# Kernel tuning notes

Measured on AMD Instinct MI355X. Metric: run time of the kernel, lower is better.

## Reference

```python
import jax, jax.numpy as jnp
import numpy as np

EPS = 1e-12  # matches torch.nn.functional.normalize default eps

def _l2_normalize(x):
    # F.normalize: x / max(||x||_2, eps)
    n = jnp.linalg.norm(x, axis=-1, keepdims=True)
    return x / jnp.maximum(n, EPS)

def setup_inputs() -> dict:
    key = jax.random.key(0)
    k_z, k_e = jax.random.split(key)
    B, N, D, K = 8, 4096, 64, 8192
    z = jax.random.normal(k_z, (B, N, D), dtype=jnp.float32)
    # nn.Embedding weight initialized uniform(-1/K, 1/K)
    embedding = jax.random.uniform(k_e, (K, D), dtype=jnp.float32,
                                   minval=-1.0 / K, maxval=1.0 / K)
    return {"z": z, "embedding": embedding, "temperature": 1.0}

def reference(z, embedding, temperature):
    z_norm = _l2_normalize(z)                      # (B,N,D)
    codebook = _l2_normalize(embedding)            # (K,D)
    sim = jnp.einsum('bnd,kd->bnk', z_norm, codebook)  # (B,N,K)
    dists = 1.0 - sim
    probs = jax.nn.softmax(-dists / temperature, axis=-1)  # (B,N,K)
    z_q = jnp.einsum('bnk,kd->bnd', probs, codebook)       # (B,N,D)
    return (probs, z_q)
```

## Files before the change

kernel.cpp:

```cpp
#include <hip/hip_runtime.h>
#include <hip/hip_bf16.h>


#define M_TOTAL 32768
#define KCODES  8192
#define DDIM    64
#define KSPLIT  4
#define KCHUNK  (KCODES / KSPLIT)

typedef __attribute__((ext_vector_type(8))) short bf16x8;
typedef __attribute__((ext_vector_type(4))) float f32x4;

__device__ inline unsigned short f2bf(float x) {
  union { float f; unsigned u; } v; v.f = x;
  unsigned r = v.u + 0x7FFFu + ((v.u >> 16) & 1u);
  return (unsigned short)(r >> 16);
}

__global__ __launch_bounds__(256) void norm_rows_kernel(
    const float* __restrict__ in, unsigned short* __restrict__ F,
    unsigned short* __restrict__ FT, int nrows) {
  int row = blockIdx.x * 4 + (threadIdx.x >> 6);
  int d = threadIdx.x & 63;
  if (row >= nrows) return;
  float x = in[(size_t)row * DDIM + d];
  float s = x * x;
  s += __shfl_xor(s, 1);  s += __shfl_xor(s, 2);  s += __shfl_xor(s, 4);
  s += __shfl_xor(s, 8);  s += __shfl_xor(s, 16); s += __shfl_xor(s, 32);
  float scale = 1.0f / fmaxf(sqrtf(s), 1e-12f);
  unsigned short b = f2bf(x * scale);
  {
    int blk = row >> 4, ml = row & 15;
    int h = d >> 5, g = (d >> 3) & 3, j = d & 7;
    F[((size_t)(blk * 2 + h)) * 512 + (g * 16 + ml) * 8 + j] = b;
  }
  if (FT) {
    int ds = d >> 4, dl = d & 15;
    int kb = row >> 5, kg = (row >> 3) & 3, kj = row & 7;
    FT[((size_t)(kb * 4 + ds)) * 512 + (kg * 16 + dl) * 8 + kj] = b;
  }
}

__global__ __launch_bounds__(512, 4) void passA_kernel(
    const unsigned short* __restrict__ FZn,
    const unsigned short* __restrict__ FCb,
    const unsigned short* __restrict__ FCbT,
    const float* __restrict__ tptr,
    float* __restrict__ Up,
    float* __restrict__ rsp) {
  __shared__ __align__(16) unsigned short sbuf[2][4096];
  __shared__ __align__(16) unsigned short etile[8][2][16 * 56];
  const int tid = threadIdx.x;
  const int w  = tid >> 6, l = tid & 63, g = l >> 4, ml = l & 15;
  const int rb = blockIdx.x & 127;
  const int ks = blockIdx.x >> 7;
  const int mA = rb * 256 + w * 32;
  const int mB = mA + 16;
  const int k0 = ks * KCHUNK;
  const float sc = 1.4426950408889634f / tptr[0];

  const unsigned short* fz = FZn + ((size_t)((rb * 16 + w * 2) * 2)) * 512;
  const bf16x8 zA0 = *(const bf16x8*)(fz + l * 8);
  const bf16x8 zA1 = *(const bf16x8*)(fz + 512 + l * 8);
  const bf16x8 zB0 = *(const bf16x8*)(fz + 1024 + l * 8);
  const bf16x8 zB1 = *(const bf16x8*)(fz + 1536 + l * 8);

  const f32x4 zero = {0.f, 0.f, 0.f, 0.f};
  f32x4 uaccA[4] = {zero, zero, zero, zero};
  f32x4 uaccB[4] = {zero, zero, zero, zero};
  float rsA = 0.f, rsB = 0.f;

  const unsigned short* gb = (tid < 256 ? FCb : FCbT) + (size_t)(tid & 255) * 8;
  bf16x8 stg = *(const bf16x8*)(gb + (size_t)k0 * 64);
  int cur = 0;

  const int NIT = KCHUNK / 32;
  for (int it = 0; it < NIT; ++it) {
    *(bf16x8*)&sbuf[cur][tid * 8] = stg;
    if (it + 1 < NIT)
      stg = *(const bf16x8*)(gb + (size_t)(k0 + (it + 1) * 32) * 64);
    __syncthreads();
    const unsigned short* sb = &sbuf[cur][0];
#pragma unroll
    for (int cs = 0; cs < 2; ++cs) {
      const bf16x8 c0 = *(const bf16x8*)(sb + cs * 1024 + l * 8);
      const bf16x8 c1 = *(const bf16x8*)(sb + cs * 1024 + 512 + l * 8);
      f32x4 aA = __builtin_amdgcn_mfma_f32_16x16x32_bf16(c0, zA0, zero, 0, 0, 0);
      aA = __builtin_amdgcn_mfma_f32_16x16x32_bf16(c1, zA1, aA, 0, 0, 0);
      f32x4 aB = __builtin_amdgcn_mfma_f32_16x16x32_bf16(c0, zB0, zero, 0, 0, 0);
      aB = __builtin_amdgcn_mfma_f32_16x16x32_bf16(c1, zB1, aB, 0, 0, 0);
      float eA0 = exp2f((aA[0] - 1.0f) * sc), eA1 = exp2f((aA[1] - 1.0f) * sc);
      float eA2 = exp2f((aA[2] - 1.0f) * sc), eA3 = exp2f((aA[3] - 1.0f) * sc);
      float eB0 = exp2f((aB[0] - 1.0f) * sc), eB1 = exp2f((aB[1] - 1.0f) * sc);
      float eB2 = exp2f((aB[2] - 1.0f) * sc), eB3 = exp2f((aB[3] - 1.0f) * sc);
      rsA += (eA0 + eA1) + (eA2 + eA3);
      rsB += (eB0 + eB1) + (eB2 + eB3);
      union { __hip_bfloat162 h[2]; uint2 u; } pA, pB;
      pA.h[0] = __float22bfloat162_rn(make_float2(eA0, eA1));
      pA.h[1] = __float22bfloat162_rn(make_float2(eA2, eA3));
      pB.h[0] = __float22bfloat162_rn(make_float2(eB0, eB1));
      pB.h[1] = __float22bfloat162_rn(make_float2(eB2, eB3));
      *(uint2*)&etile[w][0][ml * 56 + cs * 16 + g * 4] = pA.u;
      *(uint2*)&etile[w][1][ml * 56 + cs * 16 + g * 4] = pB.u;
    }
    asm volatile("s_waitcnt lgkmcnt(0)" ::: "memory");
    const bf16x8 efA = *(const bf16x8*)&etile[w][0][ml * 56 + g * 8];
    const bf16x8 efB = *(const bf16x8*)&etile[w][1][ml * 56 + g * 8];
#pragma unroll
    for (int ds = 0; ds < 4; ++ds) {
      const bf16x8 ct = *(const bf16x8*)(sb + 2048 + ds * 512 + l * 8);
      uaccA[ds] = __builtin_amdgcn_mfma_f32_16x16x32_bf16(ct, efA, uaccA[ds], 0, 0, 0);
      uaccB[ds] = __builtin_amdgcn_mfma_f32_16x16x32_bf16(ct, efB, uaccB[ds], 0, 0, 0);
    }
    cur ^= 1;
  }

  rsA += __shfl_xor(rsA, 16);  rsA += __shfl_xor(rsA, 32);
  rsB += __shfl_xor(rsB, 16);  rsB += __shfl_xor(rsB, 32);
  if (g == 0) {
    rsp[(size_t)ks * M_TOTAL + mA + ml] = rsA;
    rsp[(size_t)ks * M_TOTAL + mB + ml] = rsB;
  }

  float* urA = Up + ((size_t)ks * M_TOTAL + mA + ml) * DDIM;
  float* urB = Up + ((size_t)ks * M_TOTAL + mB + ml) * DDIM;
#pragma unroll
  for (int ds = 0; ds < 4; ++ds) {
    *(f32x4*)(urA + ds * 16 + g * 4) = uaccA[ds];
    *(f32x4*)(urB + ds * 16 + g * 4) = uaccB[ds];
  }
}

__global__ __launch_bounds__(256) void rszq_kernel(
    const float* __restrict__ Up, const float* __restrict__ rsp,
    float* __restrict__ rs, float* __restrict__ zq) {
  size_t i = (size_t)blockIdx.x * 256 + threadIdx.x;
  int m = (int)(i >> 4);
  float s = rsp[m] + rsp[M_TOTAL + m] + rsp[2 * M_TOTAL + m] + rsp[3 * M_TOTAL + m];
  if ((i & 15) == 0) rs[m] = s;
  f32x4 u = *(const f32x4*)(Up + i * 4);
#pragma unroll
  for (int ks = 1; ks < KSPLIT; ++ks) {
    f32x4 p = *(const f32x4*)(Up + (size_t)ks * M_TOTAL * DDIM + i * 4);
#pragma unroll
    for (int r = 0; r < 4; ++r) u[r] += p[r];
  }
  float inv = 1.0f / s;
  f32x4 v = {u[0] * inv, u[1] * inv, u[2] * inv, u[3] * inv};
  *(f32x4*)(zq + i * 4) = v;
}

__global__ __launch_bounds__(512, 4) void probs_kernel(
    const unsigned short* __restrict__ FZn,
    const unsigned short* __restrict__ FCb,
    const float* __restrict__ tptr,
    const float* __restrict__ rsv,
    float* __restrict__ probs) {
  __shared__ __align__(16) unsigned short sbuf[2][4096];
  const int tid = threadIdx.x;
  const int w  = tid >> 6, l = tid & 63, g = l >> 4, ml = l & 15;
  const int rb = blockIdx.x & 255;
  const int ks = blockIdx.x >> 8;
  const int m_base = rb * 128 + w * 16;
  const int k0 = ks * KCHUNK;
  const float sc = 1.4426950408889634f / tptr[0];

  const unsigned short* fz = FZn + ((size_t)((rb * 8 + w) * 2)) * 512;
  const bf16x8 zn0 = *(const bf16x8*)(fz + l * 8);
  const bf16x8 zn1 = *(const bf16x8*)(fz + 512 + l * 8);
  const float inv = 1.0f / rsv[m_base + ml];
  const f32x4 zero = {0.f, 0.f, 0.f, 0.f};
  float* prow = probs + (size_t)(m_base + ml) * KCODES;

  const unsigned short* gb = FCb + (size_t)tid * 8;
  bf16x8 stg = *(const bf16x8*)(gb + (size_t)k0 * 64);
  int cur = 0;

  const int NIT = KCHUNK / 64;
  for (int it = 0; it < NIT; ++it) {
    *(bf16x8*)&sbuf[cur][tid * 8] = stg;
    if (it + 1 < NIT)
      stg = *(const bf16x8*)(gb + (size_t)(k0 + (it + 1) * 64) * 64);
    __syncthreads();
    const unsigned short* sb = &sbuf[cur][0];
    const int kc = k0 + it * 64;
#pragma unroll
    for (int cb = 0; cb < 4; ++cb) {
      const bf16x8 c0 = *(const bf16x8*)(sb + (cb * 2 + 0) * 512 + l * 8);
      const bf16x8 c1 = *(const bf16x8*)(sb + (cb * 2 + 1) * 512 + l * 8);
      f32x4 a = __builtin_amdgcn_mfma_f32_16x16x32_bf16(c0, zn0, zero, 0, 0, 0);
      a = __builtin_amdgcn_mfma_f32_16x16x32_bf16(c1, zn1, a, 0, 0, 0);
      f32x4 p;
#pragma unroll
      for (int r = 0; r < 4; ++r) p[r] = exp2f((a[r] - 1.0f) * sc) * inv;
      *(f32x4*)(prow + kc + cb * 16 + g * 4) = p;
    }
    cur ^= 1;
  }
}

extern "C" void kernel_launch(void* const* d_in, const int* in_sizes, int n_in,
                              void* d_out, int out_size, void* d_ws, size_t ws_size,
                              hipStream_t stream) {
  const float* z    = (const float*)d_in[0];
  const float* emb  = (const float*)d_in[1];
  const float* temp = (const float*)d_in[2];

  float* probs = (float*)d_out;
  float* zq    = probs + (size_t)M_TOTAL * KCODES;

  unsigned short* FZn  = (unsigned short*)d_ws;
  unsigned short* FCb  = FZn + (size_t)M_TOTAL * DDIM;
  unsigned short* FCbT = FCb + (size_t)KCODES * DDIM;
  float* Up  = (float*)(FCbT + (size_t)KCODES * DDIM);
  float* rsp = Up + (size_t)KSPLIT * M_TOTAL * DDIM;
  float* rs  = rsp + (size_t)KSPLIT * M_TOTAL;

  norm_rows_kernel<<<M_TOTAL / 4, 256, 0, stream>>>(z, FZn, nullptr, M_TOTAL);
  norm_rows_kernel<<<KCODES / 4, 256, 0, stream>>>(emb, FCb, FCbT, KCODES);
  passA_kernel<<<128 * KSPLIT, 512, 0, stream>>>(FZn, FCb, FCbT, temp, Up, rsp);
  rszq_kernel<<<(M_TOTAL * DDIM / 4) / 256, 256, 0, stream>>>(Up, rsp, rs, zq);
  probs_kernel<<<256 * KSPLIT, 512, 0, stream>>>(FZn, FCb, temp, rs, probs);
}
```

Measured before the change: 378.6 us.

## Move probs@codebook accumulation from row-sum pass into probs-writing pass

The first pass now only computes the softmax row sums, dropping the bf16 exp tile and second MFMA product. The z_q accumulation moves into the probs pass: it reuses the already normalized probabilities, packs them to bf16 in LDS and multiplies them by the transposed codebook, so z_q no longer needs a final division. The small reduction kernel is split into a row-sum combine before the second pass and a z_q combine after it. This makes the first pass lighter and folds the z_q GEMM into a pass that is mostly limited by the probs write bandwidth. The cost is more LDS and registers in the second pass, whose launch bound drops to 2 blocks per CU.

```diff
diff --git a/kernel.cpp b/kernel.cpp
--- a/kernel.cpp
+++ b/kernel.cpp
@@ -41,15 +41,12 @@
   }
 }
 
-__global__ __launch_bounds__(512, 4) void passA_kernel(
+__global__ __launch_bounds__(512, 4) void pass1_kernel(
     const unsigned short* __restrict__ FZn,
     const unsigned short* __restrict__ FCb,
-    const unsigned short* __restrict__ FCbT,
     const float* __restrict__ tptr,
-    float* __restrict__ Up,
     float* __restrict__ rsp) {
   __shared__ __align__(16) unsigned short sbuf[2][4096];
-  __shared__ __align__(16) unsigned short etile[8][2][16 * 56];
   const int tid = threadIdx.x;
   const int w  = tid >> 6, l = tid & 63, g = l >> 4, ml = l & 15;
   const int rb = blockIdx.x & 127;
@@ -66,9 +63,77 @@
   const bf16x8 zB1 = *(const bf16x8*)(fz + 1536 + l * 8);
 
   const f32x4 zero = {0.f, 0.f, 0.f, 0.f};
-  f32x4 uaccA[4] = {zero, zero, zero, zero};
-  f32x4 uaccB[4] = {zero, zero, zero, zero};
   float rsA = 0.f, rsB = 0.f;
+
+  const unsigned short* gb = FCb + (size_t)tid * 8;
+  bf16x8 stg = *(const bf16x8*)(gb + (size_t)k0 * 64);
+  int cur = 0;
+
+  const int NIT = KCHUNK / 64;
+  for (int it = 0; it < NIT; ++it) {
+    *(bf16x8*)&sbuf[cur][tid * 8] = stg;
+    if (it + 1 < NIT)
+      stg = *(const bf16x8*)(gb + (size_t)(k0 + (it + 1) * 64) * 64);
+    __syncthreads();
+    const unsigned short* sb = &sbuf[cur][0];
+#pragma unroll
+    for (int cb = 0; cb < 4; ++cb) {
+      const bf16x8 c0 = *(const bf16x8*)(sb + cb * 1024 + l * 8);
+      const bf16x8 c1 = *(const bf16x8*)(sb + cb * 1024 + 512 + l * 8);
+      f32x4 aA = __builtin_amdgcn_mfma_f32_16x16x32_bf16(c0, zA0, zero, 0, 0, 0);
+      aA = __builtin_amdgcn_mfma_f32_16x16x32_bf16(c1, zA1, aA, 0, 0, 0);
+      f32x4 aB = __builtin_amdgcn_mfma_f32_16x16x32_bf16(c0, zB0, zero, 0, 0, 0);
+      aB = __builtin_amdgcn_mfma_f32_16x16x32_bf16(c1, zB1, aB, 0, 0, 0);
+      rsA += (exp2f((aA[0] - 1.0f) * sc) + exp2f((aA[1] - 1.0f) * sc))
+           + (exp2f((aA[2] - 1.0f) * sc) + exp2f((aA[3] - 1.0f) * sc));
+      rsB += (exp2f((aB[0] - 1.0f) * sc) + exp2f((aB[1] - 1.0f) * sc))
+           + (exp2f((aB[2] - 1.0f) * sc) + exp2f((aB[3] - 1.0f) * sc));
+    }
+    cur ^= 1;
+  }
+
+  rsA += __shfl_xor(rsA, 16);  rsA += __shfl_xor(rsA, 32);
+  rsB += __shfl_xor(rsB, 16);  rsB += __shfl_xor(rsB, 32);
+  if (g == 0) {
+    rsp[(size_t)ks * M_TOTAL + mA + ml] = rsA;
+    rsp[(size_t)ks * M_TOTAL + mB + ml] = rsB;
+  }
+}
+
+__global__ __launch_bounds__(256) void rs_kernel(
+    const float* __restrict__ rsp, float* __restrict__ rs) {
+  int m = blockIdx.x * 256 + threadIdx.x;
+  float s = 0.f;
+#pragma unroll
+  for (int ks = 0; ks < KSPLIT; ++ks) s += rsp[(size_t)ks * M_TOTAL + m];
+  rs[m] = s;
+}
+
+__global__ __launch_bounds__(512, 2) void pass2_kernel(
+    const unsigned short* __restrict__ FZn,
+    const unsigned short* __restrict__ FCb,
+    const unsigned short* __restrict__ FCbT,
+    const float* __restrict__ tptr,
+    const float* __restrict__ rsv,
+    float* __restrict__ probs,
+    float* __restrict__ Up) {
+  __shared__ __align__(16) unsigned short sbuf[2][4096];
+  __shared__ __align__(16) unsigned short etile[8][16 * 56];
+  const int tid = threadIdx.x;
+  const int w  = tid >> 6, l = tid & 63, g = l >> 4, ml = l & 15;
+  const int rb = blockIdx.x & 255;
+  const int ks = blockIdx.x >> 8;
+  const int m_base = rb * 128 + w * 16;
+  const int k0 = ks * KCHUNK;
+  const float sc = 1.4426950408889634f / tptr[0];
+
+  const unsigned short* fz = FZn + ((size_t)((rb * 8 + w) * 2)) * 512;
+  const bf16x8 zn0 = *(const bf16x8*)(fz + l * 8);
+  const bf16x8 zn1 = *(const bf16x8*)(fz + 512 + l * 8);
+  const float inv = 1.0f / rsv[m_base + ml];
+  const f32x4 zero = {0.f, 0.f, 0.f, 0.f};
+  f32x4 uacc[4] = {zero, zero, zero, zero};
+  float* prow = probs + (size_t)(m_base + ml) * KCODES;
 
   const unsigned short* gb = (tid < 256 ? FCb : FCbT) + (size_t)(tid & 255) * 8;
   bf16x8 stg = *(const bf16x8*)(gb + (size_t)k0 * 64);
@@ -81,122 +146,51 @@
       stg = *(const bf16x8*)(gb + (size_t)(k0 + (it + 1) * 32) * 64);
     __syncthreads();
     const unsigned short* sb = &sbuf[cur][0];
+    const int kc = k0 + it * 32;
 #pragma unroll
     for (int cs = 0; cs < 2; ++cs) {
       const bf16x8 c0 = *(const bf16x8*)(sb + cs * 1024 + l * 8);
       const bf16x8 c1 = *(const bf16x8*)(sb + cs * 1024 + 512 + l * 8);
-      f32x4 aA = __builtin_amdgcn_mfma_f32_16x16x32_bf16(c0, zA0, zero, 0, 0, 0);
-      aA = __builtin_amdgcn_mfma_f32_16x16x32_bf16(c1, zA1, aA, 0, 0, 0);
-      f32x4 aB = __builtin_amdgcn_mfma_f32_16x16x32_bf16(c0, zB0, zero, 0, 0, 0);
-      aB = __builtin_amdgcn_mfma_f32_16x16x32_bf16(c1, zB1, aB, 0, 0, 0);
-      float eA0 = exp2f((aA[0] - 1.0f) * sc), eA1 = exp2f((aA[1] - 1.0f) * sc);
-      float eA2 = exp2f((aA[2] - 1.0f) * sc), eA3 = exp2f((aA[3] - 1.0f) * sc);
-      float eB0 = exp2f((aB[0] - 1.0f) * sc), eB1 = exp2f((aB[1] - 1.0f) * sc);
-      float eB2 = exp2f((aB[2] - 1.0f) * sc), eB3 = exp2f((aB[3] - 1.0f) * sc);
-      rsA += (eA0 + eA1) + (eA2 + eA3);
-      rsB += (eB0 + eB1) + (eB2 + eB3);
-      union { __hip_bfloat162 h[2]; uint2 u; } pA, pB;
-      pA.h[0] = __float22bfloat162_rn(make_float2(eA0, eA1));
-      pA.h[1] = __float22bfloat162_rn(make_float2(eA2, eA3));
-      pB.h[0] = __float22bfloat162_rn(make_float2(eB0, eB1));
-      pB.h[1] = __float22bfloat162_rn(make_float2(eB2, eB3));
-      *(uint2*)&etile[w][0][ml * 56 + cs * 16 + g * 4] = pA.u;
-      *(uint2*)&etile[w][1][ml * 56 + cs * 16 + g * 4] = pB.u;
-    }
-    asm volatile("s_waitcnt lgkmcnt(0)" ::: "memory");
-    const bf16x8 efA = *(const bf16x8*)&etile[w][0][ml * 56 + g * 8];
-    const bf16x8 efB = *(const bf16x8*)&etile[w][1][ml * 56 + g * 8];
-#pragma unroll
-    for (int ds = 0; ds < 4; ++ds) {
-      const bf16x8 ct = *(const bf16x8*)(sb + 2048 + ds * 512 + l * 8);
-      uaccA[ds] = __builtin_amdgcn_mfma_f32_16x16x32_bf16(ct, efA, uaccA[ds], 0, 0, 0);
-      uaccB[ds] = __builtin_amdgcn_mfma_f32_16x16x32_bf16(ct, efB, uaccB[ds], 0, 0, 0);
-    }
-    cur ^= 1;
-  }
-
-  rsA += __shfl_xor(rsA, 16);  rsA += __shfl_xor(rsA, 32);
-  rsB += __shfl_xor(rsB, 16);  rsB += __shfl_xor(rsB, 32);
-  if (g == 0) {
-    rsp[(size_t)ks * M_TOTAL + mA + ml] = rsA;
-    rsp[(size_t)ks * M_TOTAL + mB + ml] = rsB;
-  }
-
-  float* urA = Up + ((size_t)ks * M_TOTAL + mA + ml) * DDIM;
-  float* urB = Up + ((size_t)ks * M_TOTAL + mB + ml) * DDIM;
-#pragma unroll
-  for (int ds = 0; ds < 4; ++ds) {
-    *(f32x4*)(urA + ds * 16 + g * 4) = uaccA[ds];
-    *(f32x4*)(urB + ds * 16 + g * 4) = uaccB[ds];
-  }
-}
-
-__global__ __launch_bounds__(256) void rszq_kernel(
-    const float* __restrict__ Up, const float* __restrict__ rsp,
-    float* __restrict__ rs, float* __restrict__ zq) {
-  size_t i = (size_t)blockIdx.x * 256 + threadIdx.x;
-  int m = (int)(i >> 4);
-  float s = rsp[m] + rsp[M_TOTAL + m] + rsp[2 * M_TOTAL + m] + rsp[3 * M_TOTAL + m];
-  if ((i & 15) == 0) rs[m] = s;
-  f32x4 u = *(const f32x4*)(Up + i * 4);
-#pragma unroll
-  for (int ks = 1; ks < KSPLIT; ++ks) {
-    f32x4 p = *(const f32x4*)(Up + (size_t)ks * M_TOTAL * DDIM + i * 4);
-#pragma unroll
-    for (int r = 0; r < 4; ++r) u[r] += p[r];
-  }
-  float inv = 1.0f / s;
-  f32x4 v = {u[0] * inv, u[1] * inv, u[2] * inv, u[3] * inv};
-  *(f32x4*)(zq + i * 4) = v;
-}
-
-__global__ __launch_bounds__(512, 4) void probs_kernel(
-    const unsigned short* __restrict__ FZn,
-    const unsigned short* __restrict__ FCb,
-    const float* __restrict__ tptr,
-    const float* __restrict__ rsv,
-    float* __restrict__ probs) {
-  __shared__ __align__(16) unsigned short sbuf[2][4096];
-  const int tid = threadIdx.x;
-  const int w  = tid >> 6, l = tid & 63, g = l >> 4, ml = l & 15;
-  const int rb = blockIdx.x & 255;
-  const int ks = blockIdx.x >> 8;
-  const int m_base = rb * 128 + w * 16;
-  const int k0 = ks * KCHUNK;
-  const float sc = 1.4426950408889634f / tptr[0];
-
-  const unsigned short* fz = FZn + ((size_t)((rb * 8 + w) * 2)) * 512;
-  const bf16x8 zn0 = *(const bf16x8*)(fz + l * 8);
-  const bf16x8 zn1 = *(const bf16x8*)(fz + 512 + l * 8);
-  const float inv = 1.0f / rsv[m_base + ml];
-  const f32x4 zero = {0.f, 0.f, 0.f, 0.f};
-  float* prow = probs + (size_t)(m_base + ml) * KCODES;
-
-  const unsigned short* gb = FCb + (size_t)tid * 8;
-  bf16x8 stg = *(const bf16x8*)(gb + (size_t)k0 * 64);
-  int cur = 0;
-
-  const int NIT = KCHUNK / 64;
-  for (int it = 0; it < NIT; ++it) {
-    *(bf16x8*)&sbuf[cur][tid * 8] = stg;
-    if (it + 1 < NIT)
-      stg = *(const bf16x8*)(gb + (size_t)(k0 + (it + 1) * 64) * 64);
-    __syncthreads();
-    const unsigned short* sb = &sbuf[cur][0];
-    const int kc = k0 + it * 64;
-#pragma unroll
-    for (int cb = 0; cb < 4; ++cb) {
-      const bf16x8 c0 = *(const bf16x8*)(sb + (cb * 2 + 0) * 512 + l * 8);
-      const bf16x8 c1 = *(const bf16x8*)(sb + (cb * 2 + 1) * 512 + l * 8);
       f32x4 a = __builtin_amdgcn_mfma_f32_16x16x32_bf16(c0, zn0, zero, 0, 0, 0);
       a = __builtin_amdgcn_mfma_f32_16x16x32_bf16(c1, zn1, a, 0, 0, 0);
       f32x4 p;
-#pragma unroll
-      for (int r = 0; r < 4; ++r) p[r] = exp2f((a[r] - 1.0f) * sc) * inv;
-      *(f32x4*)(prow + kc + cb * 16 + g * 4) = p;
+      p[0] = exp2f((a[0] - 1.0f) * sc) * inv;
+      p[1] = exp2f((a[1] - 1.0f) * sc) * inv;
+      p[2] = exp2f((a[2] - 1.0f) * sc) * inv;
+      p[3] = exp2f((a[3] - 1.0f) * sc) * inv;
+      *(f32x4*)(prow + kc + cs * 16 + g * 4) = p;
+      union { __hip_bfloat162 h[2]; uint2 u; } pk;
+      pk.h[0] = __float22bfloat162_rn(make_float2(p[0], p[1]));
+      pk.h[1] = __float22bfloat162_rn(make_float2(p[2], p[3]));
+      *(uint2*)&etile[w][ml * 56 + cs * 16 + g * 4] = pk.u;
+    }
+    asm volatile("s_waitcnt lgkmcnt(0)" ::: "memory");
+    const bf16x8 ef = *(const bf16x8*)&etile[w][ml * 56 + g * 8];
+#pragma unroll
+    for (int ds = 0; ds < 4; ++ds) {
+      const bf16x8 ct = *(const bf16x8*)(sb + 2048 + ds * 512 + l * 8);
+      uacc[ds] = __builtin_amdgcn_mfma_f32_16x16x32_bf16(ct, ef, uacc[ds], 0, 0, 0);
     }
     cur ^= 1;
   }
+
+  float* urow = Up + ((size_t)ks * M_TOTAL + m_base + ml) * DDIM;
+#pragma unroll
+  for (int ds = 0; ds < 4; ++ds)
+    *(f32x4*)(urow + ds * 16 + g * 4) = uacc[ds];
+}
+
+__global__ __launch_bounds__(256) void zq_kernel(
+    const float* __restrict__ Up, float* __restrict__ zq) {
+  size_t i = (size_t)blockIdx.x * 256 + threadIdx.x;
+  f32x4 u = *(const f32x4*)(Up + i * 4);
+#pragma unroll
+  for (int ks = 1; ks < KSPLIT; ++ks) {
+    f32x4 p = *(const f32x4*)(Up + (size_t)ks * M_TOTAL * DDIM + i * 4);
+#pragma unroll
+    for (int r = 0; r < 4; ++r) u[r] += p[r];
+  }
+  *(f32x4*)(zq + i * 4) = u;
 }
 
 extern "C" void kernel_launch(void* const* d_in, const int* in_sizes, int n_in,
@@ -218,7 +212,8 @@
 
   norm_rows_kernel<<<M_TOTAL / 4, 256, 0, stream>>>(z, FZn, nullptr, M_TOTAL);
   norm_rows_kernel<<<KCODES / 4, 256, 0, stream>>>(emb, FCb, FCbT, KCODES);
-  passA_kernel<<<128 * KSPLIT, 512, 0, stream>>>(FZn, FCb, FCbT, temp, Up, rsp);
-  rszq_kernel<<<(M_TOTAL * DDIM / 4) / 256, 256, 0, stream>>>(Up, rsp, rs, zq);
-  probs_kernel<<<256 * KSPLIT, 512, 0, stream>>>(FZn, FCb, temp, rs, probs);
-}
+  pass1_kernel<<<128 * KSPLIT, 512, 0, stream>>>(FZn, FCb, temp, rsp);
+  rs_kernel<<<M_TOTAL / 256, 256, 0, stream>>>(rsp, rs);
+  pass2_kernel<<<256 * KSPLIT, 512, 0, stream>>>(FZn, FCb, FCbT, temp, rs, probs, Up);
+  zq_kernel<<<(M_TOTAL * DDIM / 4) / 256, 256, 0, stream>>>(Up, zq);
+}
```

Measured after the change: 368.5 us. -2.7%, faster.
